# Performance work log

Hardware: AMD Instinct MI355X
Metric: run time of the kernel (lower is better)

Reference implementation:

```python
import jax, jax.numpy as jnp
import numpy as np

N_NODES = 100000
N_EDGES = 3200000
F_IN = 256
N_CLASSES = 10


def setup_inputs() -> dict:
    key = jax.random.key(0)
    ks = jax.random.split(key, 10)
    x = jax.random.normal(ks[0], (N_NODES, F_IN), dtype=jnp.float32)
    edge_index = jax.random.randint(ks[1], (2, N_EDGES), 0, N_NODES, dtype=jnp.int64)
    def glorot(k, fan_in, fan_out):
        s = (6.0 / (fan_in + fan_out)) ** 0.5
        return jax.random.uniform(k, (fan_in, fan_out), jnp.float32, -s, s)
    return {
        "x": x,
        "edge_index": edge_index,
        "W_gcn": glorot(ks[2], F_IN, 64),
        "b_gcn": jnp.zeros((64,), jnp.float32),
        "W1": glorot(ks[3], 64, 32),
        "b1": jnp.zeros((32,), jnp.float32),
        "W2": glorot(ks[4], 32, 16),
        "b2": jnp.zeros((16,), jnp.float32),
        "W3": glorot(ks[5], 16, N_CLASSES),
        "b3": jnp.zeros((N_CLASSES,), jnp.float32),
    }


def gcn_conv(x, edge_index, W, b):
    # PyG GCNConv: x' = D^{-1/2} (A + I) D^{-1/2} (x W) + b, with self-loops.
    n = x.shape[0]
    loop = jnp.arange(n, dtype=edge_index.dtype)
    src = jnp.concatenate([edge_index[0], loop])  # [E+N]
    dst = jnp.concatenate([edge_index[1], loop])
    deg = jax.ops.segment_sum(jnp.ones(src.shape, jnp.float32), dst, num_segments=n)
    dinv = jnp.where(deg > 0, jax.lax.rsqrt(deg), 0.0)
    norm = dinv[src] * dinv[dst]  # [E+N]
    h = x @ W  # transform first (reduces message width to 64)
    msg = h[src] * norm[:, None]  # gather + scale
    out = jax.ops.segment_sum(msg, dst, num_segments=n)  # scatter-add
    return out + b


def reference(x, edge_index, W_gcn, b_gcn, W1, b1, W2, b2, W3, b3):
    # Dropout is a no-op in eval mode; reference uses deterministic eval math.
    h = jax.nn.relu(gcn_conv(x, edge_index, W_gcn, b_gcn))
    h = jax.nn.relu(h @ W1 + b1)
    h = jax.nn.relu(h @ W2 + b2)
    return h @ W3 + b3
```

## Files before the change

### kernel.cpp

```cpp
#include <hip/hip_runtime.h>

#define F_IN 256
#define CHUNK 8192
#define CAP 10240

typedef short bf8_t __attribute__((ext_vector_type(8)));
typedef float f4_t  __attribute__((ext_vector_type(4)));

__device__ __forceinline__ unsigned short f2bf(float f) {
  unsigned u = __float_as_uint(f);
  unsigned r = (u + 0x7FFFu + ((u >> 16) & 1u)) >> 16;
  return (unsigned short)r;
}
#define BF_LO(d) __uint_as_float((d) << 16)
#define BF_HI(d) __uint_as_float((d) & 0xFFFF0000u)

__device__ __forceinline__ bf8_t pack8(float4 a, float4 b) {
  bf8_t r;
  r[0] = (short)f2bf(a.x); r[1] = (short)f2bf(a.y);
  r[2] = (short)f2bf(a.z); r[3] = (short)f2bf(a.w);
  r[4] = (short)f2bf(b.x); r[5] = (short)f2bf(b.y);
  r[6] = (short)f2bf(b.z); r[7] = (short)f2bf(b.w);
  return r;
}

__global__ __launch_bounds__(256) void wprep_kernel(
    const float* __restrict__ W, unsigned short* __restrict__ WbT,
    unsigned short* __restrict__ hb, int N) {
  const int t = threadIdx.x;
  const int i = blockIdx.x * 256 + t;
  const int k = i >> 6, n = i & 63;
  WbT[n * 256 + k] = f2bf(W[i]);
  if (blockIdx.x == 0 && t < 64) hb[(size_t)N * 64 + t] = 0;
}

__global__ __launch_bounds__(256) void gemm_direct_kernel(
    const float* __restrict__ x, const unsigned short* __restrict__ WbT,
    const int* __restrict__ deg, unsigned short* __restrict__ hb, int M) {
  __shared__ short Bs[64][264];
  const int t = threadIdx.x;
  for (int i = t; i < 2048; i += 256) {
    const int n = i >> 5, kq = (i & 31) << 3;
    *(uint4*)&Bs[n][kq] = *(const uint4*)(WbT + n * 256 + kq);
  }
  __syncthreads();

  const int brow = blockIdx.x * 128;
  const int w = t >> 6;
  const int l = t & 63;
  const int ml = l & 15;
  const int quad = l >> 4;

  const int r0 = min(brow + w * 32 + ml, M - 1);
  const int r1 = min(brow + w * 32 + 16 + ml, M - 1);
  const float* xr0 = x + (size_t)r0 * F_IN + (quad << 3);
  const float* xr1 = x + (size_t)r1 * F_IN + (quad << 3);

  f4_t acc[2][4];
#pragma unroll
  for (int a = 0; a < 2; ++a)
#pragma unroll
    for (int b = 0; b < 4; ++b) acc[a][b] = (f4_t){0.f, 0.f, 0.f, 0.f};

#pragma unroll
  for (int k0 = 0; k0 < F_IN; k0 += 32) {
    bf8_t afr[2];
    {
      const float4 a0 = *(const float4*)(xr0 + k0);
      const float4 a1 = *(const float4*)(xr0 + k0 + 4);
      afr[0] = pack8(a0, a1);
      const float4 c0 = *(const float4*)(xr1 + k0);
      const float4 c1 = *(const float4*)(xr1 + k0 + 4);
      afr[1] = pack8(c0, c1);
    }
    bf8_t bfr[4];
#pragma unroll
    for (int nt = 0; nt < 4; ++nt)
      bfr[nt] = *(const bf8_t*)&Bs[nt * 16 + ml][k0 + (quad << 3)];
#pragma unroll
    for (int mt = 0; mt < 2; ++mt)
#pragma unroll
      for (int nt = 0; nt < 4; ++nt)
        acc[mt][nt] = __builtin_amdgcn_mfma_f32_16x16x32_bf16(
            afr[mt], bfr[nt], acc[mt][nt], 0, 0, 0);
  }

#pragma unroll
  for (int mt = 0; mt < 2; ++mt) {
#pragma unroll
    for (int reg = 0; reg < 4; ++reg) {
      const int row = brow + w * 32 + mt * 16 + (quad << 2) + reg;
      if (row < M) {
        const float di = rsqrtf((float)deg[row] + 1.f);
#pragma unroll
        for (int nt = 0; nt < 4; ++nt)
          hb[(size_t)row * 64 + nt * 16 + ml] = f2bf(di * acc[mt][nt][reg]);
      }
    }
  }
}

__global__ __launch_bounds__(512) void sort_local_kernel(
    const int* __restrict__ src_arr, const int* __restrict__ dst_arr,
    int* __restrict__ espB, int* __restrict__ segStart, int* __restrict__ segCnt,
    int E, int NBK) {
  __shared__ int hist[512];
  __shared__ int s[512];
  __shared__ int cur[512];
  const int t = threadIdx.x;
  const int blk = blockIdx.x;
  const int base = blk * CHUNK;
  const int cnt = min(CHUNK, E - base);
  for (int i = t; i < NBK; i += 512) hist[i] = 0;
  __syncthreads();
  int pk[16], bk[16];
#pragma unroll
  for (int k = 0; k < 16; ++k) {
    const int i = t + k * 512;
    bk[k] = -1;
    if (i < cnt) {
      const int sv = src_arr[base + i];
      const int dv = dst_arr[base + i];
      pk[k] = sv | ((dv & 255) << 24);
      bk[k] = dv >> 8;
      atomicAdd(&hist[bk[k]], 1);
    }
  }
  __syncthreads();
  const int v = (t < NBK) ? hist[t] : 0;
  s[t] = v;
  __syncthreads();
#pragma unroll
  for (int off = 1; off < 512; off <<= 1) {
    int add = (t >= off) ? s[t - off] : 0;
    __syncthreads();
    s[t] += add;
    __syncthreads();
  }
  if (t < NBK) {
    const int excl = s[t] - v;
    cur[t] = excl;
    segStart[blk * NBK + t] = base + excl;
    segCnt[blk * NBK + t] = v;
  }
  __syncthreads();
#pragma unroll
  for (int k = 0; k < 16; ++k) {
    if (bk[k] >= 0) {
      const int pos = atomicAdd(&cur[bk[k]], 1);
      espB[base + pos] = pk[k];
    }
  }
}

__global__ __launch_bounds__(512) void deg_hist_kernel(
    const int* __restrict__ espB, const int* __restrict__ segStart,
    const int* __restrict__ segCnt, int* __restrict__ deg,
    int N, int NBK, int NCH) {
  __shared__ int segS[512];
  __shared__ int segC[512];
  __shared__ int hist[256];
  const int t = threadIdx.x;
  const int b = blockIdx.x;
  segS[t] = 0;
  segC[t] = 0;
  if (t < 256) hist[t] = 0;
  __syncthreads();
  for (int i = t; i < NCH; i += 512) {
    segS[i] = segStart[i * NBK + b];
    segC[i] = segCnt[i * NBK + b];
  }
  __syncthreads();
  const int sw = t >> 4, sl = t & 15;
  for (int seg = sw; seg < NCH; seg += 32) {
    const int sS = segS[seg], c = segC[seg];
    for (int j = sl; j < c; j += 16)
      atomicAdd(&hist[((unsigned)espB[sS + j]) >> 24], 1);
  }
  __syncthreads();
  if (t < 256) {
    const int node = b * 256 + t;
    if (node < N) deg[node] = hist[t];
  }
}

__global__ __launch_bounds__(512) void bin_agg_kernel(
    const int* __restrict__ espB, const int* __restrict__ segStart,
    const int* __restrict__ segCnt, const int* __restrict__ deg,
    const unsigned short* __restrict__ hb, const float* __restrict__ bg,
    unsigned short* __restrict__ g, int N, int NBK, int NCH) {
  __shared__ int eLDS[CAP];
  __shared__ int segS[512];
  __shared__ int segC[512];
  __shared__ int sbuf[256];
  __shared__ int hist[256];
  __shared__ int cur[256];
  __shared__ int stt[256];
  const int t = threadIdx.x;
  const int b = blockIdx.x;
  segS[t] = 0;
  segC[t] = 0;
  __syncthreads();
  for (int i = t; i < NCH; i += 512) {
    segS[i] = segStart[i * NBK + b];
    segC[i] = segCnt[i * NBK + b];
  }
  int v2 = 0, vp = 0;
  if (t < 256) {
    const int node = b * 256 + t;
    v2 = (node < N) ? deg[node] : 0;
    vp = (v2 + 3) & ~3;
    sbuf[t] = vp;
  }
  __syncthreads();
#pragma unroll
  for (int off = 1; off < 256; off <<= 1) {
    int add = 0;
    if (t < 256 && t >= off) add = sbuf[t - off];
    __syncthreads();
    if (t < 256) sbuf[t] += add;
    __syncthreads();
  }
  if (t < 256) {
    const int excl = sbuf[t] - vp;
    cur[t] = excl;
    stt[t] = excl;
    hist[t] = v2;
  }
  __syncthreads();

  const int sw = t >> 4;
  const int sl = t & 15;

  for (int seg = sw; seg < NCH; seg += 32) {
    const int sS = segS[seg], c = segC[seg];
    for (int j = sl; j < c; j += 16) {
      const int p = espB[sS + j];
      const int pos = atomicAdd(&cur[((unsigned)p) >> 24], 1);
      if (pos < CAP) eLDS[pos] = p & 0x00FFFFFF;
    }
  }
  __syncthreads();
  if (t < 256) {
    const int e0 = cur[t];
    const int e1 = stt[t] + ((hist[t] + 3) & ~3);
    for (int i2 = e0; i2 < e1 && i2 < CAP; ++i2) eLDS[i2] = N;
  }
  __syncthreads();

  const int w = t >> 6;
  const int lane = t & 63;
  const int gi = lane >> 3;
  const int fq = (lane & 7) << 3;

#pragma unroll
  for (int p = 0; p < 4; ++p) {
    const int ln = p * 64 + w * 8 + gi;
    const int node = b * 256 + ln;
    const int cn = hist[ln];
    const int start = stt[ln];
    const int R = (cn + 3) >> 2;

    float acc[8] = {0.f, 0.f, 0.f, 0.f, 0.f, 0.f, 0.f, 0.f};
    int i = start;
    int s0 = 0, s1 = 0, s2 = 0, s3 = 0;
    if (R > 0) { s0 = eLDS[i]; s1 = eLDS[i + 1]; s2 = eLDS[i + 2]; s3 = eLDS[i + 3]; }
    for (int r = 0; r < R; ++r) {
      const uint4 r0 = *(const uint4*)(hb + (size_t)s0 * 64 + fq);
      const uint4 r1 = *(const uint4*)(hb + (size_t)s1 * 64 + fq);
      const uint4 r2 = *(const uint4*)(hb + (size_t)s2 * 64 + fq);
      const uint4 r3 = *(const uint4*)(hb + (size_t)s3 * 64 + fq);
      i += 4;
      if (r + 1 < R) { s0 = eLDS[i]; s1 = eLDS[i + 1]; s2 = eLDS[i + 2]; s3 = eLDS[i + 3]; }
      acc[0] += (BF_LO(r0.x) + BF_LO(r1.x)) + (BF_LO(r2.x) + BF_LO(r3.x));
      acc[1] += (BF_HI(r0.x) + BF_HI(r1.x)) + (BF_HI(r2.x) + BF_HI(r3.x));
      acc[2] += (BF_LO(r0.y) + BF_LO(r1.y)) + (BF_LO(r2.y) + BF_LO(r3.y));
      acc[3] += (BF_HI(r0.y) + BF_HI(r1.y)) + (BF_HI(r2.y) + BF_HI(r3.y));
      acc[4] += (BF_LO(r0.z) + BF_LO(r1.z)) + (BF_LO(r2.z) + BF_LO(r3.z));
      acc[5] += (BF_HI(r0.z) + BF_HI(r1.z)) + (BF_HI(r2.z) + BF_HI(r3.z));
      acc[6] += (BF_LO(r0.w) + BF_LO(r1.w)) + (BF_LO(r2.w) + BF_LO(r3.w));
      acc[7] += (BF_HI(r0.w) + BF_HI(r1.w)) + (BF_HI(r2.w) + BF_HI(r3.w));
    }

    if (node < N) {
      const float di = rsqrtf((float)(cn + 1));
      const uint4 rr = *(const uint4*)(hb + (size_t)node * 64 + fq);
      const float4 bq0 = *(const float4*)(bg + fq);
      const float4 bq1 = *(const float4*)(bg + fq + 4);
      float4 v0 = make_float4(
          fmaxf(di * (acc[0] + BF_LO(rr.x)) + bq0.x, 0.f),
          fmaxf(di * (acc[1] + BF_HI(rr.x)) + bq0.y, 0.f),
          fmaxf(di * (acc[2] + BF_LO(rr.y)) + bq0.z, 0.f),
          fmaxf(di * (acc[3] + BF_HI(rr.y)) + bq0.w, 0.f));
      float4 v1 = make_float4(
          fmaxf(di * (acc[4] + BF_LO(rr.z)) + bq1.x, 0.f),
          fmaxf(di * (acc[5] + BF_HI(rr.z)) + bq1.y, 0.f),
          fmaxf(di * (acc[6] + BF_LO(rr.w)) + bq1.z, 0.f),
          fmaxf(di * (acc[7] + BF_HI(rr.w)) + bq1.w, 0.f));
      *(bf8_t*)(g + (size_t)node * 64 + fq) = pack8(v0, v1);
    }
  }
}

__global__ __launch_bounds__(256) void mlp_mfma_kernel(
    const unsigned short* __restrict__ g,
    const float* __restrict__ W1, const float* __restrict__ b1,
    const float* __restrict__ W2, const float* __restrict__ b2,
    const float* __restrict__ W3, const float* __restrict__ b3,
    float* __restrict__ out, int N) {
  __shared__ short g64[256 * 72];
  __shared__ short h2s[256 * 40];
  __shared__ short W1s[32 * 72];
  __shared__ short W2s[16 * 40];
  __shared__ short W3s[16 * 40];
  __shared__ float b1s[32], b2s[16], b3s[16];
  short* h1s = g64;

  const int t = threadIdx.x;
  const int node0 = blockIdx.x * 256;
  for (int i = t; i < 256 * 40; i += 256) h2s[i] = 0;
  for (int i = t; i < 16 * 40; i += 256) W3s[i] = 0;
  if (t < 32) b1s[t] = b1[t];
  if (t < 16) { b2s[t] = b2[t]; b3s[t] = (t < 10) ? b3[t] : 0.f; }
  __syncthreads();
  for (int i = t; i < 2048; i += 256) { const int k = i >> 5, n = i & 31; W1s[n * 72 + k] = (short)f2bf(W1[i]); }
  for (int i = t; i < 512;  i += 256) { const int k = i >> 4, n = i & 15; W2s[n * 40 + k] = (short)f2bf(W2[i]); }
  if (t < 160) { const int k = t / 10, n = t % 10; W3s[n * 40 + k] = (short)f2bf(W3[t]); }
  for (int i = t; i < 2048; i += 256) {
    const int row = i >> 3, q = (i & 7) << 3;
    const int nd = min(node0 + row, N - 1);
    *(uint4*)&g64[row * 72 + q] = *(const uint4*)(g + (size_t)nd * 64 + q);
  }
  __syncthreads();

  const int w = t >> 6;
  const int lane = t & 63;
  const int ml = lane & 15;
  const int quad = lane >> 4;

  bf8_t a1f[4][2], b1f[2][2];
#pragma unroll
  for (int mt = 0; mt < 4; ++mt)
#pragma unroll
    for (int ks = 0; ks < 2; ++ks)
      a1f[mt][ks] = *(const bf8_t*)&g64[(w * 64 + mt * 16 + ml) * 72 + ks * 32 + quad * 8];
#pragma unroll
  for (int nt = 0; nt < 2; ++nt)
#pragma unroll
    for (int ks = 0; ks < 2; ++ks)
      b1f[nt][ks] = *(const bf8_t*)&W1s[(nt * 16 + ml) * 72 + ks * 32 + quad * 8];
  f4_t acc1[4][2];
#pragma unroll
  for (int mt = 0; mt < 4; ++mt)
#pragma unroll
    for (int nt = 0; nt < 2; ++nt) acc1[mt][nt] = (f4_t){0.f, 0.f, 0.f, 0.f};
#pragma unroll
  for (int ks = 0; ks < 2; ++ks)
#pragma unroll
    for (int mt = 0; mt < 4; ++mt)
#pragma unroll
      for (int nt = 0; nt < 2; ++nt)
        acc1[mt][nt] = __builtin_amdgcn_mfma_f32_16x16x32_bf16(
            a1f[mt][ks], b1f[nt][ks], acc1[mt][nt], 0, 0, 0);
  __syncthreads();
#pragma unroll
  for (int mt = 0; mt < 4; ++mt)
#pragma unroll
    for (int nt = 0; nt < 2; ++nt)
#pragma unroll
      for (int reg = 0; reg < 4; ++reg) {
        const int row = w * 64 + mt * 16 + quad * 4 + reg;
        const int col = nt * 16 + ml;
        h1s[row * 40 + col] = (short)f2bf(fmaxf(acc1[mt][nt][reg] + b1s[col], 0.f));
      }
  __syncthreads();

  bf8_t a2f[4];
#pragma unroll
  for (int mt = 0; mt < 4; ++mt)
    a2f[mt] = *(const bf8_t*)&h1s[(w * 64 + mt * 16 + ml) * 40 + quad * 8];
  const bf8_t b2f = *(const bf8_t*)&W2s[ml * 40 + quad * 8];
  f4_t acc2[4];
#pragma unroll
  for (int mt = 0; mt < 4; ++mt) {
    acc2[mt] = (f4_t){0.f, 0.f, 0.f, 0.f};
    acc2[mt] = __builtin_amdgcn_mfma_f32_16x16x32_bf16(a2f[mt], b2f, acc2[mt], 0, 0, 0);
  }
  __syncthreads();
#pragma unroll
  for (int mt = 0; mt < 4; ++mt)
#pragma unroll
    for (int reg = 0; reg < 4; ++reg) {
      const int row = w * 64 + mt * 16 + quad * 4 + reg;
      h2s[row * 40 + ml] = (short)f2bf(fmaxf(acc2[mt][reg] + b2s[ml], 0.f));
    }
  __syncthreads();

  bf8_t a3f[4];
#pragma unroll
  for (int mt = 0; mt < 4; ++mt)
    a3f[mt] = *(const bf8_t*)&h2s[(w * 64 + mt * 16 + ml) * 40 + quad * 8];
  const bf8_t b3f = *(const bf8_t*)&W3s[ml * 40 + quad * 8];
#pragma unroll
  for (int mt = 0; mt < 4; ++mt) {
    f4_t acc3 = (f4_t){0.f, 0.f, 0.f, 0.f};
    acc3 = __builtin_amdgcn_mfma_f32_16x16x32_bf16(a3f[mt], b3f, acc3, 0, 0, 0);
#pragma unroll
    for (int reg = 0; reg < 4; ++reg) {
      const int node = node0 + w * 64 + mt * 16 + quad * 4 + reg;
      if (ml < 10 && node < N) out[(size_t)node * 10 + ml] = acc3[reg] + b3s[ml];
    }
  }
}

extern "C" void kernel_launch(void* const* d_in, const int* in_sizes, int n_in,
                              void* d_out, int out_size, void* d_ws, size_t ws_size,
                              hipStream_t stream) {
  const float* x     = (const float*)d_in[0];
  const int*   ei    = (const int*)d_in[1];
  const float* W_gcn = (const float*)d_in[2];
  const float* b_gcn = (const float*)d_in[3];
  const float* W1    = (const float*)d_in[4];
  const float* b1    = (const float*)d_in[5];
  const float* W2    = (const float*)d_in[6];
  const float* b2    = (const float*)d_in[7];
  const float* W3    = (const float*)d_in[8];
  const float* b3    = (const float*)d_in[9];
  float* out = (float*)d_out;

  const int N = in_sizes[0] / F_IN;
  const int E = in_sizes[1] / 2;
  const int* src = ei;
  const int* dst = ei + E;
  const int NBK = (N + 255) >> 8;
  const int NCH = (E + CHUNK - 1) / CHUNK;

  unsigned short* hb = (unsigned short*)d_ws;
  int*   deg         = (int*)(hb + (size_t)(N + 1) * 64);
  int*   espB        = deg + N;
  int*   segStart    = espB + E;
  int*   segCnt      = segStart + NCH * NBK;
  unsigned short* WbT= (unsigned short*)(segCnt + NCH * NBK);
  unsigned short* g  = WbT + 16384;

  wprep_kernel<<<64, 256, 0, stream>>>(W_gcn, WbT, hb, N);
  sort_local_kernel<<<NCH, 512, 0, stream>>>(
      src, dst, espB, segStart, segCnt, E, NBK);
  deg_hist_kernel<<<NBK, 512, 0, stream>>>(
      espB, segStart, segCnt, deg, N, NBK, NCH);

  gemm_direct_kernel<<<(N + 127) / 128, 256, 0, stream>>>(x, WbT, deg, hb, N);

  bin_agg_kernel<<<NBK, 512, 0, stream>>>(
      espB, segStart, segCnt, deg, hb, b_gcn, g, N, NBK, NCH);

  mlp_mfma_kernel<<<(N + 255) / 256, 256, 0, stream>>>(
      g, W1, b1, W2, b2, W3, b3, out, N);
}
```

Before: 300.3 us.

## Fuse GCN aggregation with MLP head into one kernel sharing LDS

Merges the bin aggregation kernel and the three-layer MFMA MLP kernel into a single kernel. Aggregated node features now stay in LDS, reusing the edge-list buffer, instead of being written to global memory as bf16 and read back. This removes one launch and a global round trip. The MLP now runs across 8 waves with 32 rows each, and all four accumulator sets are held in registers at once, which adds register pressure. The espB reads also switch to nontemporal loads.

```diff
diff --git a/kernel.cpp b/kernel.cpp
--- a/kernel.cpp
+++ b/kernel.cpp
@@ -175,7 +175,7 @@
   for (int seg = sw; seg < NCH; seg += 32) {
     const int sS = segS[seg], c = segC[seg];
     for (int j = sl; j < c; j += 16)
-      atomicAdd(&hist[((unsigned)espB[sS + j]) >> 24], 1);
+      atomicAdd(&hist[((unsigned)__builtin_nontemporal_load(espB + sS + j)) >> 24], 1);
   }
   __syncthreads();
   if (t < 256) {
@@ -184,27 +184,46 @@
   }
 }
 
-__global__ __launch_bounds__(512) void bin_agg_kernel(
+__global__ __launch_bounds__(512) void bin_agg_mlp_kernel(
     const int* __restrict__ espB, const int* __restrict__ segStart,
     const int* __restrict__ segCnt, const int* __restrict__ deg,
     const unsigned short* __restrict__ hb, const float* __restrict__ bg,
-    unsigned short* __restrict__ g, int N, int NBK, int NCH) {
-  __shared__ int eLDS[CAP];
-  __shared__ int segS[512];
-  __shared__ int segC[512];
+    const float* __restrict__ W1, const float* __restrict__ b1,
+    const float* __restrict__ W2, const float* __restrict__ b2,
+    const float* __restrict__ W3, const float* __restrict__ b3,
+    float* __restrict__ out, int N, int NBK, int NCH) {
+  __shared__ int lds_pool[CAP + 1024];
+  __shared__ short h2s[256 * 40];
+  __shared__ short W1s[32 * 72];
+  __shared__ short W2s[16 * 40];
+  __shared__ short W3s[16 * 40];
+  __shared__ float b1s[32], b2s[16], b3s[16];
   __shared__ int sbuf[256];
   __shared__ int hist[256];
   __shared__ int cur[256];
   __shared__ int stt[256];
+  int* eLDS = lds_pool;
+  int* segS = lds_pool + CAP;
+  int* segC = lds_pool + CAP + 512;
+  short* g64 = (short*)lds_pool;
+  short* h1s = g64;
+
   const int t = threadIdx.x;
   const int b = blockIdx.x;
-  segS[t] = 0;
-  segC[t] = 0;
+  if (t < 512) { segS[t] = 0; segC[t] = 0; }
+  for (int i = t; i < 256 * 40; i += 512) h2s[i] = 0;
+  for (int i = t; i < 16 * 40; i += 512) W3s[i] = 0;
+  if (t < 32) b1s[t] = b1[t];
+  if (t < 16) { b2s[t] = b2[t]; b3s[t] = (t < 10) ? b3[t] : 0.f; }
   __syncthreads();
   for (int i = t; i < NCH; i += 512) {
     segS[i] = segStart[i * NBK + b];
     segC[i] = segCnt[i * NBK + b];
   }
+  for (int i = t; i < 2048; i += 512) { const int k = i >> 5, n = i & 31; W1s[n * 72 + k] = (short)f2bf(W1[i]); }
+  for (int i = t; i < 512;  i += 512) { const int k = i >> 4, n = i & 15; W2s[n * 40 + k] = (short)f2bf(W2[i]); }
+  if (t < 160) { const int k = t / 10, n = t % 10; W3s[n * 40 + k] = (short)f2bf(W3[t]); }
+
   int v2 = 0, vp = 0;
   if (t < 256) {
     const int node = b * 256 + t;
@@ -235,7 +254,7 @@
   for (int seg = sw; seg < NCH; seg += 32) {
     const int sS = segS[seg], c = segC[seg];
     for (int j = sl; j < c; j += 16) {
-      const int p = espB[sS + j];
+      const int p = __builtin_nontemporal_load(espB + sS + j);
       const int pos = atomicAdd(&cur[((unsigned)p) >> 24], 1);
       if (pos < CAP) eLDS[pos] = p & 0x00FFFFFF;
     }
@@ -253,15 +272,19 @@
   const int gi = lane >> 3;
   const int fq = (lane & 7) << 3;
 
+  float accA[4][8];
+#pragma unroll
+  for (int p = 0; p < 4; ++p)
+#pragma unroll
+    for (int j = 0; j < 8; ++j) accA[p][j] = 0.f;
+
 #pragma unroll
   for (int p = 0; p < 4; ++p) {
     const int ln = p * 64 + w * 8 + gi;
-    const int node = b * 256 + ln;
     const int cn = hist[ln];
     const int start = stt[ln];
     const int R = (cn + 3) >> 2;
 
-    float acc[8] = {0.f, 0.f, 0.f, 0.f, 0.f, 0.f, 0.f, 0.f};
     int i = start;
     int s0 = 0, s1 = 0, s2 = 0, s3 = 0;
     if (R > 0) { s0 = eLDS[i]; s1 = eLDS[i + 1]; s2 = eLDS[i + 2]; s3 = eLDS[i + 3]; }
@@ -272,142 +295,115 @@
       const uint4 r3 = *(const uint4*)(hb + (size_t)s3 * 64 + fq);
       i += 4;
       if (r + 1 < R) { s0 = eLDS[i]; s1 = eLDS[i + 1]; s2 = eLDS[i + 2]; s3 = eLDS[i + 3]; }
-      acc[0] += (BF_LO(r0.x) + BF_LO(r1.x)) + (BF_LO(r2.x) + BF_LO(r3.x));
-      acc[1] += (BF_HI(r0.x) + BF_HI(r1.x)) + (BF_HI(r2.x) + BF_HI(r3.x));
-      acc[2] += (BF_LO(r0.y) + BF_LO(r1.y)) + (BF_LO(r2.y) + BF_LO(r3.y));
-      acc[3] += (BF_HI(r0.y) + BF_HI(r1.y)) + (BF_HI(r2.y) + BF_HI(r3.y));
-      acc[4] += (BF_LO(r0.z) + BF_LO(r1.z)) + (BF_LO(r2.z) + BF_LO(r3.z));
-      acc[5] += (BF_HI(r0.z) + BF_HI(r1.z)) + (BF_HI(r2.z) + BF_HI(r3.z));
-      acc[6] += (BF_LO(r0.w) + BF_LO(r1.w)) + (BF_LO(r2.w) + BF_LO(r3.w));
-      acc[7] += (BF_HI(r0.w) + BF_HI(r1.w)) + (BF_HI(r2.w) + BF_HI(r3.w));
-    }
-
-    if (node < N) {
-      const float di = rsqrtf((float)(cn + 1));
-      const uint4 rr = *(const uint4*)(hb + (size_t)node * 64 + fq);
-      const float4 bq0 = *(const float4*)(bg + fq);
-      const float4 bq1 = *(const float4*)(bg + fq + 4);
-      float4 v0 = make_float4(
-          fmaxf(di * (acc[0] + BF_LO(rr.x)) + bq0.x, 0.f),
-          fmaxf(di * (acc[1] + BF_HI(rr.x)) + bq0.y, 0.f),
-          fmaxf(di * (acc[2] + BF_LO(rr.y)) + bq0.z, 0.f),
-          fmaxf(di * (acc[3] + BF_HI(rr.y)) + bq0.w, 0.f));
-      float4 v1 = make_float4(
-          fmaxf(di * (acc[4] + BF_LO(rr.z)) + bq1.x, 0.f),
-          fmaxf(di * (acc[5] + BF_HI(rr.z)) + bq1.y, 0.f),
-          fmaxf(di * (acc[6] + BF_LO(rr.w)) + bq1.z, 0.f),
-          fmaxf(di * (acc[7] + BF_HI(rr.w)) + bq1.w, 0.f));
-      *(bf8_t*)(g + (size_t)node * 64 + fq) = pack8(v0, v1);
-    }
-  }
-}
-
-__global__ __launch_bounds__(256) void mlp_mfma_kernel(
-    const unsigned short* __restrict__ g,
-    const float* __restrict__ W1, const float* __restrict__ b1,
-    const float* __restrict__ W2, const float* __restrict__ b2,
-    const float* __restrict__ W3, const float* __restrict__ b3,
-    float* __restrict__ out, int N) {
-  __shared__ short g64[256 * 72];
-  __shared__ short h2s[256 * 40];
-  __shared__ short W1s[32 * 72];
-  __shared__ short W2s[16 * 40];
-  __shared__ short W3s[16 * 40];
-  __shared__ float b1s[32], b2s[16], b3s[16];
-  short* h1s = g64;
-
-  const int t = threadIdx.x;
-  const int node0 = blockIdx.x * 256;
-  for (int i = t; i < 256 * 40; i += 256) h2s[i] = 0;
-  for (int i = t; i < 16 * 40; i += 256) W3s[i] = 0;
-  if (t < 32) b1s[t] = b1[t];
-  if (t < 16) { b2s[t] = b2[t]; b3s[t] = (t < 10) ? b3[t] : 0.f; }
-  __syncthreads();
-  for (int i = t; i < 2048; i += 256) { const int k = i >> 5, n = i & 31; W1s[n * 72 + k] = (short)f2bf(W1[i]); }
-  for (int i = t; i < 512;  i += 256) { const int k = i >> 4, n = i & 15; W2s[n * 40 + k] = (short)f2bf(W2[i]); }
-  if (t < 160) { const int k = t / 10, n = t % 10; W3s[n * 40 + k] = (short)f2bf(W3[t]); }
-  for (int i = t; i < 2048; i += 256) {
-    const int row = i >> 3, q = (i & 7) << 3;
-    const int nd = min(node0 + row, N - 1);
-    *(uint4*)&g64[row * 72 + q] = *(const uint4*)(g + (size_t)nd * 64 + q);
-  }
-  __syncthreads();
-
-  const int w = t >> 6;
-  const int lane = t & 63;
+      accA[p][0] += (BF_LO(r0.x) + BF_LO(r1.x)) + (BF_LO(r2.x) + BF_LO(r3.x));
+      accA[p][1] += (BF_HI(r0.x) + BF_HI(r1.x)) + (BF_HI(r2.x) + BF_HI(r3.x));
+      accA[p][2] += (BF_LO(r0.y) + BF_LO(r1.y)) + (BF_LO(r2.y) + BF_LO(r3.y));
+      accA[p][3] += (BF_HI(r0.y) + BF_HI(r1.y)) + (BF_HI(r2.y) + BF_HI(r3.y));
+      accA[p][4] += (BF_LO(r0.z) + BF_LO(r1.z)) + (BF_LO(r2.z) + BF_LO(r3.z));
+      accA[p][5] += (BF_HI(r0.z) + BF_HI(r1.z)) + (BF_HI(r2.z) + BF_HI(r3.z));
+      accA[p][6] += (BF_LO(r0.w) + BF_LO(r1.w)) + (BF_LO(r2.w) + BF_LO(r3.w));
+      accA[p][7] += (BF_HI(r0.w) + BF_HI(r1.w)) + (BF_HI(r2.w) + BF_HI(r3.w));
+    }
+  }
+  __syncthreads();
+
+#pragma unroll
+  for (int p = 0; p < 4; ++p) {
+    const int ln = p * 64 + w * 8 + gi;
+    const int node = b * 256 + ln;
+    const int cn = hist[ln];
+    const float di = rsqrtf((float)(cn + 1));
+    const int selfRow = min(node, N);
+    const uint4 rr = *(const uint4*)(hb + (size_t)selfRow * 64 + fq);
+    const float4 bq0 = *(const float4*)(bg + fq);
+    const float4 bq1 = *(const float4*)(bg + fq + 4);
+    float4 v0 = make_float4(
+        fmaxf(di * (accA[p][0] + BF_LO(rr.x)) + bq0.x, 0.f),
+        fmaxf(di * (accA[p][1] + BF_HI(rr.x)) + bq0.y, 0.f),
+        fmaxf(di * (accA[p][2] + BF_LO(rr.y)) + bq0.z, 0.f),
+        fmaxf(di * (accA[p][3] + BF_HI(rr.y)) + bq0.w, 0.f));
+    float4 v1 = make_float4(
+        fmaxf(di * (accA[p][4] + BF_LO(rr.z)) + bq1.x, 0.f),
+        fmaxf(di * (accA[p][5] + BF_HI(rr.z)) + bq1.y, 0.f),
+        fmaxf(di * (accA[p][6] + BF_LO(rr.w)) + bq1.z, 0.f),
+        fmaxf(di * (accA[p][7] + BF_HI(rr.w)) + bq1.w, 0.f));
+    *(bf8_t*)&g64[ln * 72 + fq] = pack8(v0, v1);
+  }
+  __syncthreads();
+
   const int ml = lane & 15;
   const int quad = lane >> 4;
 
-  bf8_t a1f[4][2], b1f[2][2];
-#pragma unroll
-  for (int mt = 0; mt < 4; ++mt)
+  bf8_t a1f[2][2], b1f[2][2];
+#pragma unroll
+  for (int mt = 0; mt < 2; ++mt)
 #pragma unroll
     for (int ks = 0; ks < 2; ++ks)
-      a1f[mt][ks] = *(const bf8_t*)&g64[(w * 64 + mt * 16 + ml) * 72 + ks * 32 + quad * 8];
+      a1f[mt][ks] = *(const bf8_t*)&g64[(w * 32 + mt * 16 + ml) * 72 + ks * 32 + quad * 8];
 #pragma unroll
   for (int nt = 0; nt < 2; ++nt)
 #pragma unroll
     for (int ks = 0; ks < 2; ++ks)
       b1f[nt][ks] = *(const bf8_t*)&W1s[(nt * 16 + ml) * 72 + ks * 32 + quad * 8];
-  f4_t acc1[4][2];
-#pragma unroll
-  for (int mt = 0; mt < 4; ++mt)
+  f4_t acc1[2][2];
+#pragma unroll
+  for (int mt = 0; mt < 2; ++mt)
 #pragma unroll
     for (int nt = 0; nt < 2; ++nt) acc1[mt][nt] = (f4_t){0.f, 0.f, 0.f, 0.f};
 #pragma unroll
   for (int ks = 0; ks < 2; ++ks)
 #pragma unroll
-    for (int mt = 0; mt < 4; ++mt)
+    for (int mt = 0; mt < 2; ++mt)
 #pragma unroll
       for (int nt = 0; nt < 2; ++nt)
         acc1[mt][nt] = __builtin_amdgcn_mfma_f32_16x16x32_bf16(
             a1f[mt][ks], b1f[nt][ks], acc1[mt][nt], 0, 0, 0);
   __syncthreads();
 #pragma unroll
-  for (int mt = 0; mt < 4; ++mt)
+  for (int mt = 0; mt < 2; ++mt)
 #pragma unroll
     for (int nt = 0; nt < 2; ++nt)
 #pragma unroll
       for (int reg = 0; reg < 4; ++reg) {
-        const int row = w * 64 + mt * 16 + quad * 4 + reg;
+        const int row = w * 32 + mt * 16 + quad * 4 + reg;
         const int col = nt * 16 + ml;
         h1s[row * 40 + col] = (short)f2bf(fmaxf(acc1[mt][nt][reg] + b1s[col], 0.f));
       }
   __syncthreads();
 
-  bf8_t a2f[4];
-#pragma unroll
-  for (int mt = 0; mt < 4; ++mt)
-    a2f[mt] = *(const bf8_t*)&h1s[(w * 64 + mt * 16 + ml) * 40 + quad * 8];
+  bf8_t a2f[2];
+#pragma unroll
+  for (int mt = 0; mt < 2; ++mt)
+    a2f[mt] = *(const bf8_t*)&h1s[(w * 32 + mt * 16 + ml) * 40 + quad * 8];
   const bf8_t b2f = *(const bf8_t*)&W2s[ml * 40 + quad * 8];
-  f4_t acc2[4];
-#pragma unroll
-  for (int mt = 0; mt < 4; ++mt) {
+  f4_t acc2[2];
+#pragma unroll
+  for (int mt = 0; mt < 2; ++mt) {
     acc2[mt] = (f4_t){0.f, 0.f, 0.f, 0.f};
     acc2[mt] = __builtin_amdgcn_mfma_f32_16x16x32_bf16(a2f[mt], b2f, acc2[mt], 0, 0, 0);
   }
   __syncthreads();
 #pragma unroll
-  for (int mt = 0; mt < 4; ++mt)
+  for (int mt = 0; mt < 2; ++mt)
 #pragma unroll
     for (int reg = 0; reg < 4; ++reg) {
-      const int row = w * 64 + mt * 16 + quad * 4 + reg;
+      const int row = w * 32 + mt * 16 + quad * 4 + reg;
       h2s[row * 40 + ml] = (short)f2bf(fmaxf(acc2[mt][reg] + b2s[ml], 0.f));
     }
   __syncthreads();
 
-  bf8_t a3f[4];
-#pragma unroll
-  for (int mt = 0; mt < 4; ++mt)
-    a3f[mt] = *(const bf8_t*)&h2s[(w * 64 + mt * 16 + ml) * 40 + quad * 8];
+  bf8_t a3f[2];
+#pragma unroll
+  for (int mt = 0; mt < 2; ++mt)
+    a3f[mt] = *(const bf8_t*)&h2s[(w * 32 + mt * 16 + ml) * 40 + quad * 8];
   const bf8_t b3f = *(const bf8_t*)&W3s[ml * 40 + quad * 8];
 #pragma unroll
-  for (int mt = 0; mt < 4; ++mt) {
+  for (int mt = 0; mt < 2; ++mt) {
     f4_t acc3 = (f4_t){0.f, 0.f, 0.f, 0.f};
     acc3 = __builtin_amdgcn_mfma_f32_16x16x32_bf16(a3f[mt], b3f, acc3, 0, 0, 0);
 #pragma unroll
     for (int reg = 0; reg < 4; ++reg) {
-      const int node = node0 + w * 64 + mt * 16 + quad * 4 + reg;
+      const int node = b * 256 + w * 32 + mt * 16 + quad * 4 + reg;
       if (ml < 10 && node < N) out[(size_t)node * 10 + ml] = acc3[reg] + b3s[ml];
     }
   }
@@ -441,7 +437,6 @@
   int*   segStart    = espB + E;
   int*   segCnt      = segStart + NCH * NBK;
   unsigned short* WbT= (unsigned short*)(segCnt + NCH * NBK);
-  unsigned short* g  = WbT + 16384;
 
   wprep_kernel<<<64, 256, 0, stream>>>(W_gcn, WbT, hb, N);
   sort_local_kernel<<<NCH, 512, 0, stream>>>(
@@ -451,9 +446,7 @@
 
   gemm_direct_kernel<<<(N + 127) / 128, 256, 0, stream>>>(x, WbT, deg, hb, N);
 
-  bin_agg_kernel<<<NBK, 512, 0, stream>>>(
-      espB, segStart, segCnt, deg, hb, b_gcn, g, N, NBK, NCH);
-
-  mlp_mfma_kernel<<<(N + 255) / 256, 256, 0, stream>>>(
-      g, W1, b1, W2, b2, W3, b3, out, N);
-}
+  bin_agg_mlp_kernel<<<NBK, 512, 0, stream>>>(
+      espB, segStart, segCnt, deg, hb, b_gcn,
+      W1, b1, W2, b2, W3, b3, out, N, NBK, NCH);
+}
```

Result: no change. 303.1 us (+0.9%).
